# Kernel optimization log

Hardware: AMD Instinct MI355X
Metric: run time of the kernel (lower is better)

Reference implementation:

```python
import jax, jax.numpy as jnp
import numpy as np

K = 16          # nodes_num
BN_EPS = 1e-5


def _bn_conv_relu(x, w, gamma, beta, mean, var):
    # 1x1 conv on [N,K,C] node features == matmul, then eval-mode BN + ReLU
    y = jnp.einsum('nkc,oc->nko', x, w)                      # [N,K,256]
    y = (y - mean) * jax.lax.rsqrt(var + BN_EPS) * gamma + beta
    return jax.nn.relu(y)


def _lnorm(r, c):
    # Symmetric-normalized affinity from node pixel coordinates.
    # A_ij = 1/(1+||p_i-p_j||), self-loops A_ii=1, Lnorm = D^-1/2 A D^-1/2
    p = jnp.stack([r, c], axis=-1).astype(jnp.float32)        # [N,K,2]
    diff = p[:, :, None, :] - p[:, None, :, :]
    dist = jnp.sqrt(jnp.sum(diff * diff, axis=-1))            # [N,K,K]
    A = 1.0 / (1.0 + dist)
    dinv = jax.lax.rsqrt(jnp.sum(A, axis=-1))                 # [N,K]
    return A * dinv[:, :, None] * dinv[:, None, :]


def setup_inputs() -> dict:
    key = jax.random.key(0)
    ks = jax.random.split(key, 12)
    N, C, W, H = 128, 1024, 14, 14
    O = 256
    inp = {
        'fpam_output': jax.random.normal(ks[0], (N, C, W, H), jnp.float32),
        'resnet_output': jax.random.normal(ks[1], (N, 2048), jnp.float32),
        'w_max': jax.random.normal(ks[2], (O, C), jnp.float32) * 0.02,
        'g_max': 1.0 + 0.1 * jax.random.normal(ks[3], (O,), jnp.float32),
        'b_max': 0.1 * jax.random.normal(ks[4], (O,), jnp.float32),
        'm_max': 0.1 * jax.random.normal(ks[5], (O,), jnp.float32),
        'v_max': jax.random.uniform(ks[6], (O,), jnp.float32, 0.5, 1.5),
        'w_med': jax.random.normal(ks[7], (O, C), jnp.float32) * 0.02,
        'g_med': 1.0 + 0.1 * jax.random.normal(ks[8], (O,), jnp.float32),
        'b_med': 0.1 * jax.random.normal(ks[9], (O,), jnp.float32),
        'm_med': 0.1 * jax.random.normal(ks[10], (O,), jnp.float32),
        'v_med': jax.random.uniform(ks[11], (O,), jnp.float32, 0.5, 1.5),
    }
    return inp


def reference(fpam_output, resnet_output, w_max, g_max, b_max, m_max, v_max,
              w_med, g_med, b_med, m_med, v_med):
    N, C, W, H = fpam_output.shape
    HW = W * H
    # channel-sum saliency, sort descending
    fre = jnp.sum(fpam_output, axis=1).reshape(N, HW)         # [N,HW]
    idx = jnp.argsort(-fre, axis=1)
    maxK = idx[:, :K]
    mstart = HW // 2 - K // 2 - 1
    medK = idx[:, mstart:mstart + K]
    scene = jnp.concatenate([maxK, medK], axis=1)             # [N,2K]
    rows = scene // H
    cols = scene % H
    # batched gather replacing the per-pixel python loop
    flat = fpam_output.reshape(N, C, HW)
    nodes = jnp.take_along_axis(flat, scene[:, None, :], axis=2)  # [N,C,2K]
    nodes = jnp.transpose(nodes, (0, 2, 1))                   # [N,2K,C]
    x_max = _bn_conv_relu(nodes[:, :K], w_max, g_max, b_max, m_max, v_max)
    x_med = _bn_conv_relu(nodes[:, K:], w_med, g_med, b_med, m_med, v_med)
    Ltop = _lnorm(rows[:, :K], cols[:, :K])
    Lmed = _lnorm(rows[:, K:], cols[:, K:])
    max_graph = jnp.einsum('nij,njc->nic', Ltop, x_max).reshape(N, -1)
    med_graph = jnp.einsum('nij,njc->nic', Lmed, x_med).reshape(N, -1)
    return (max_graph, med_graph, rows, cols)
```

## Files before the change

kernel.cpp:

```cpp
#include <hip/hip_runtime.h>

#define NB 128
#define CC 1024
#define HWP 196
#define HH 14
#define OO 256

typedef unsigned short ushort_t;
typedef __attribute__((ext_vector_type(8))) short short8;
typedef __attribute__((ext_vector_type(4))) float float4v;

__device__ __forceinline__ ushort_t f2bf(float v) {
  union { float f; unsigned int u; } c; c.f = v;
  unsigned int u = c.u;
  unsigned int r = (u + 0x7FFFu + ((u >> 16) & 1u)) >> 16;
  return (ushort_t)r;
}

__global__ __launch_bounds__(256) void k_prep(const float* __restrict__ x,
                                              const float* __restrict__ wmax,
                                              const float* __restrict__ wmed,
                                              float* __restrict__ partial,
                                              ushort_t* __restrict__ wb) {
  const int b = blockIdx.x, t = threadIdx.x;
  if (b >= 256) {
    int idx = (b - 256) * 256 + t;
    int z = idx >> 18;
    int r = idx & (OO * CC - 1);
    const float* w = z ? wmed : wmax;
    wb[idx] = f2bf(w[r]);
    return;
  }
  const int unit = b * 4 + (t >> 6);
  const int lane = t & 63;
  if (lane >= 49) return;
  const int n = unit >> 3, cg = unit & 7;
  const float4* base = (const float4*)(x + ((size_t)n * CC + (size_t)cg * 128) * HWP);
  float4 s = {0.f, 0.f, 0.f, 0.f};
  #pragma unroll 16
  for (int c = 0; c < 128; ++c) {
    float4 v = base[c * 49 + lane];
    s.x += v.x; s.y += v.y; s.z += v.z; s.w += v.w;
  }
  ((float4*)(partial + ((size_t)n * 8 + cg) * HWP))[lane] = s;
}

__global__ __launch_bounds__(512, 2) void k_main(
    const float* __restrict__ x, const float* __restrict__ partial,
    const ushort_t* __restrict__ wb,
    const float* __restrict__ g_max, const float* __restrict__ b_max,
    const float* __restrict__ m_max, const float* __restrict__ v_max,
    const float* __restrict__ g_med, const float* __restrict__ b_med,
    const float* __restrict__ m_med, const float* __restrict__ v_med,
    float* __restrict__ out) {
  constexpr int AP = 1032;
  __shared__ alignas(16) ushort_t A_sh[16 * AP];
  __shared__ float fre[HWP];
  __shared__ int sc[32];
  __shared__ float Lsh[16][17];
  __shared__ float dinv[16];
  __shared__ float y_sh[16][257];

  const int n = blockIdx.x;
  const int z = blockIdx.y;
  const int t = threadIdx.x;

  if (t < HWP) {
    float s = 0.f;
    #pragma unroll
    for (int g = 0; g < 8; ++g) s += partial[((size_t)n * 8 + g) * HWP + t];
    fre[t] = s;
  }
  __syncthreads();
  if (t < HWP) {
    float v = fre[t];
    int rank = 0;
    #pragma unroll 4
    for (int q = 0; q < HWP; ++q) {
      float u = fre[q];
      rank += ((u > v) || (u == v && q < t)) ? 1 : 0;
    }
    if (rank < 16) sc[rank] = t;
    else if (rank >= 89 && rank < 105) sc[rank - 73] = t;
  }
  __syncthreads();

  if (z == 0 && t < 32) {
    int p = sc[t];
    out[2 * NB * 4096 + n * 32 + t] = (float)(p / HH);
    out[2 * NB * 4096 + NB * 32 + n * 32 + t] = (float)(p % HH);
  }

  {
    const int j = t & 15;
    const int g = t >> 4;
    const int sj = sc[z * 16 + j];
    const float* xb = x + (size_t)n * (CC * HWP) + (size_t)g * 32 * HWP + sj;
    ushort_t* arow = &A_sh[j * AP + g * 32];
    #pragma unroll 16
    for (int u = 0; u < 32; ++u) {
      arow[u] = f2bf(xb[(size_t)u * HWP]);
    }
  }
  if (t < 256) {
    const int i = t >> 4, j = t & 15;
    int pi = sc[z * 16 + i], pj = sc[z * 16 + j];
    float dr = (float)(pi / HH - pj / HH);
    float dc = (float)(pi % HH - pj % HH);
    Lsh[i][j] = 1.0f / (1.0f + sqrtf(dr * dr + dc * dc));
  }
  __syncthreads();
  if (t < 16) {
    float s = 0.f;
    #pragma unroll
    for (int j = 0; j < 16; ++j) s += Lsh[t][j];
    dinv[t] = rsqrtf(s);
  }

  const int w = t >> 6;
  const int l = t & 63;
  const int m = l & 15;
  const int quad = l >> 4;

  const ushort_t* Arow = &A_sh[m * AP + quad * 8];
  const ushort_t* B0 = wb + (size_t)z * (OO * CC) + (size_t)(w * 32 + m) * CC + quad * 8;

  float4v acc0 = {0.f, 0.f, 0.f, 0.f};
  float4v acc1 = acc0;

  __syncthreads();

  #pragma unroll 4
  for (int k0 = 0; k0 < CC; k0 += 32) {
    short8 a  = *reinterpret_cast<const short8*>(Arow + k0);
    short8 b0 = *reinterpret_cast<const short8*>(B0 + k0);
    short8 b1 = *reinterpret_cast<const short8*>(B0 + 16 * CC + k0);
    acc0 = __builtin_amdgcn_mfma_f32_16x16x32_bf16(a, b0, acc0, 0, 0, 0);
    acc1 = __builtin_amdgcn_mfma_f32_16x16x32_bf16(a, b1, acc1, 0, 0, 0);
  }

  const float* gp = z ? g_med : g_max;
  const float* bp = z ? b_med : b_max;
  const float* mp = z ? m_med : m_max;
  const float* vp = z ? v_med : v_max;

  #pragma unroll
  for (int tt = 0; tt < 2; ++tt) {
    float4v av = tt ? acc1 : acc0;
    int o = w * 32 + tt * 16 + m;
    float scale = gp[o] * rsqrtf(vp[o] + 1e-5f);
    float shift = bp[o] - mp[o] * scale;
    #pragma unroll
    for (int r = 0; r < 4; ++r) {
      int j = quad * 4 + r;
      float y = av[r] * scale + shift;
      y = fmaxf(y, 0.f);
      y_sh[j][o] = y * dinv[j];
    }
  }
  __syncthreads();

  {
    const int o = t & 255;
    const int ih = (t >> 8) * 8;
    float yp[16];
    #pragma unroll
    for (int j = 0; j < 16; ++j) yp[j] = y_sh[j][o];
    float* ob = out + (size_t)z * (NB * 4096) + (size_t)n * 4096 + o;
    #pragma unroll
    for (int i2 = 0; i2 < 8; ++i2) {
      const int i = ih + i2;
      float s = 0.f;
      #pragma unroll
      for (int j = 0; j < 16; ++j) s = fmaf(Lsh[i][j], yp[j], s);
      ob[(size_t)i * OO] = s * dinv[i];
    }
  }
}

extern "C" void kernel_launch(void* const* d_in, const int* in_sizes, int n_in,
                              void* d_out, int out_size, void* d_ws, size_t ws_size,
                              hipStream_t stream) {
  const float* x     = (const float*)d_in[0];
  const float* w_max = (const float*)d_in[2];
  const float* g_max = (const float*)d_in[3];
  const float* b_max = (const float*)d_in[4];
  const float* m_max = (const float*)d_in[5];
  const float* v_max = (const float*)d_in[6];
  const float* w_med = (const float*)d_in[7];
  const float* g_med = (const float*)d_in[8];
  const float* b_med = (const float*)d_in[9];
  const float* m_med = (const float*)d_in[10];
  const float* v_med = (const float*)d_in[11];
  float* out = (float*)d_out;

  float* ws_f = (float*)d_ws;
  float* partial  = ws_f;
  ushort_t* wb    = (ushort_t*)(ws_f + 200704);

  k_prep<<<dim3(256 + 2048), 256, 0, stream>>>(x, w_max, w_med, partial, wb);
  k_main<<<dim3(NB, 2), 512, 0, stream>>>(x, partial, wb,
                                          g_max, b_max, m_max, v_max,
                                          g_med, b_med, m_med, v_med, out);
}
```

Baseline: 208.3 us.

## Pre-transpose input to pixel-major bf16 so node gather reads contiguous rows

Adds 1024 blocks to the prep kernel that transpose the full input tensor through LDS into a [N, HW, C] bf16 workspace. The main kernel then gathers each selected node's 1024 channels as contiguous 16-byte loads instead of strided scalar fp32 loads with a 196-element stride. The cost is re-reading the whole 103 MB input and writing a 51 MB transposed copy, although only 32 of 196 pixels per sample are ever used. That extra traffic could outweigh the savings from the cheaper gather.

```diff
diff --git a/kernel.cpp b/kernel.cpp
--- a/kernel.cpp
+++ b/kernel.cpp
@@ -21,8 +21,36 @@
                                               const float* __restrict__ wmax,
                                               const float* __restrict__ wmed,
                                               float* __restrict__ partial,
-                                              ushort_t* __restrict__ wb) {
+                                              ushort_t* __restrict__ wb,
+                                              ushort_t* __restrict__ xT) {
   const int b = blockIdx.x, t = threadIdx.x;
+  if (b >= 2304) {
+    __shared__ alignas(16) float lds_t[32 * 200];
+    const int u2 = b - 2304;
+    const int n = u2 >> 3, cg = u2 & 7;
+    for (int ch = 0; ch < 4; ++ch) {
+      const float4* src = (const float4*)(x + ((size_t)n * CC + (size_t)cg * 128 + ch * 32) * HWP);
+      __syncthreads();
+      for (int idx = t; idx < 32 * 49; idx += 256) {
+        int r = idx / 49, q = idx - r * 49;
+        *(float4*)&lds_t[r * 200 + q * 4] = src[idx];
+      }
+      __syncthreads();
+      if (t < HWP) {
+        const int p = t;
+        ushort_t* dst = xT + ((size_t)n * HWP + p) * CC + cg * 128 + ch * 32;
+        #pragma unroll
+        for (int c8 = 0; c8 < 4; ++c8) {
+          union { short8 v; ushort_t s[8]; } pk;
+          #pragma unroll
+          for (int e = 0; e < 8; ++e)
+            pk.s[e] = f2bf(lds_t[(c8 * 8 + e) * 200 + p]);
+          *reinterpret_cast<short8*>(dst + c8 * 8) = pk.v;
+        }
+      }
+    }
+    return;
+  }
   if (b >= 256) {
     int idx = (b - 256) * 256 + t;
     int z = idx >> 18;
@@ -46,7 +74,7 @@
 }
 
 __global__ __launch_bounds__(512, 2) void k_main(
-    const float* __restrict__ x, const float* __restrict__ partial,
+    const ushort_t* __restrict__ xT, const float* __restrict__ partial,
     const ushort_t* __restrict__ wb,
     const float* __restrict__ g_max, const float* __restrict__ b_max,
     const float* __restrict__ m_max, const float* __restrict__ v_max,
@@ -92,15 +120,15 @@
   }
 
   {
-    const int j = t & 15;
-    const int g = t >> 4;
+    const int j = t >> 5;
+    const int g = t & 31;
     const int sj = sc[z * 16 + j];
-    const float* xb = x + (size_t)n * (CC * HWP) + (size_t)g * 32 * HWP + sj;
-    ushort_t* arow = &A_sh[j * AP + g * 32];
-    #pragma unroll 16
-    for (int u = 0; u < 32; ++u) {
-      arow[u] = f2bf(xb[(size_t)u * HWP]);
-    }
+    const ushort_t* src = xT + ((size_t)n * HWP + sj) * CC + g * 32;
+    ushort_t* dst = &A_sh[j * AP + g * 32];
+    #pragma unroll
+    for (int u = 0; u < 4; ++u)
+      *reinterpret_cast<short8*>(dst + u * 8) =
+          *reinterpret_cast<const short8*>(src + u * 8);
   }
   if (t < 256) {
     const int i = t >> 4, j = t & 15;
@@ -197,9 +225,11 @@
   float* ws_f = (float*)d_ws;
   float* partial  = ws_f;
   ushort_t* wb    = (ushort_t*)(ws_f + 200704);
-
-  k_prep<<<dim3(256 + 2048), 256, 0, stream>>>(x, w_max, w_med, partial, wb);
-  k_main<<<dim3(NB, 2), 512, 0, stream>>>(x, partial, wb,
+  ushort_t* xT    = (ushort_t*)(ws_f + 462848);
+
+  k_prep<<<dim3(256 + 2048 + 1024), 256, 0, stream>>>(x, w_max, w_med,
+                                                      partial, wb, xT);
+  k_main<<<dim3(NB, 2), 512, 0, stream>>>(xT, partial, wb,
                                           g_max, b_max, m_max, v_max,
                                           g_med, b_med, m_med, v_med, out);
 }
```

Measured after the change: 227.7 us. +9.3%, slower.
